# Kernel tuning notes

Hardware: AMD Instinct MI355X
Metric: run time of the kernel (lower is better)

The kernel has to match this reference:

```python
import jax, jax.numpy as jnp
import numpy as np

B, N, T = 2, 207, 864
L = 12           # patch_size
D = 96           # embed_dim
EPS = 1e-8
TAU = 1.0


def setup_inputs() -> dict:
    key = jax.random.key(0)
    k1, k2, k3, k4, k5 = jax.random.split(key, 5)
    return {
        "long_term_history": jax.random.normal(k1, (B, N, 1, T), dtype=jnp.float32),
        "adj_mx": jax.random.uniform(k2, (N, N), dtype=jnp.float32),
        "uniform_noise": jax.random.uniform(k3, (N, N), dtype=jnp.float32),
        "conv_weight": jax.random.normal(k4, (D, N, L), dtype=jnp.float32) * 0.02,
        "conv_bias": jax.random.normal(k5, (D,), dtype=jnp.float32) * 0.02,
        "k": 10,
    }


def _sample_k_neighbor_soft(adj_mx, uniform_noise, k):
    n = adj_mx.shape[0]
    logits = jnp.log(jax.nn.relu(adj_mx) + EPS)
    gumbel = -jnp.log(-jnp.log(uniform_noise + EPS))
    soft = jax.nn.softmax((logits + gumbel) / TAU, axis=1)          # [N, N]
    _, topk_idx = jax.lax.top_k(soft, k)                             # [N, k]
    hard = jnp.zeros_like(soft).at[jnp.arange(n)[:, None], topk_idx].set(1.0)
    return soft * hard                                               # [N, N]


def reference(long_term_history, adj_mx, uniform_noise, conv_weight, conv_bias, k):
    b, n, _, t = long_term_history.shape
    p = t // L
    mask = _sample_k_neighbor_soft(adj_mx, uniform_noise, k)         # [N, N]
    # expanded_history[b,i,j,t] = x[b,i,0,t]; neighbors = mask[i,j] * x[b,i,0,t]
    x = long_term_history[:, :, 0, :]                                # [B, N, T]
    neighbors = mask[None, :, :, None] * x[:, :, None, :]            # [B, N, N, T] (dense blow-up, as in source)
    xp = neighbors.reshape(b, n, n, p, L)                            # split T -> P patches of length L
    # Conv2d(N -> D, kernel (L,1), stride (L,1)) == contraction over (neighbor channel j, in-patch l)
    out = jnp.einsum('bijpl,djl->bidp', xp, conv_weight) + conv_bias[None, None, :, None]
    return out                                                       # [B, N, D, P]
```

## Files before the change

kernel.cpp:

```cpp
#include <hip/hip_runtime.h>
#include <math.h>

#define NN 207
#define BB 2
#define TT 864
#define LL 12
#define DD 96
#define PP 72
#define EPSF 1e-8f

__global__ __launch_bounds__(256) void stpe_fused_kernel(
    const float* __restrict__ x,
    const float* __restrict__ adj,
    const float* __restrict__ noise,
    const float* __restrict__ W,
    const float* __restrict__ bias,
    const int*   __restrict__ kptr,
    float*       __restrict__ out)
{
    __shared__ float s_score[NN];
    __shared__ float s_x[BB][TT];
    __shared__ float s_weff[DD * LL];
    __shared__ float s_bias[DD];
    __shared__ float s_topS[32];
    __shared__ int   s_topI[32];

    const int i   = blockIdx.x;
    const int tid = threadIdx.x;
    const int kk  = min(*kptr, 32);

    if (tid < NN) {
        float a = fmaxf(adj[i * NN + tid], 0.0f) + EPSF;
        float u = noise[i * NN + tid] + EPSF;
        s_score[tid] = logf(a) - logf(-logf(u));
    }
    if (tid < DD) s_bias[tid] = bias[tid];

    {
        const float4* x4  = (const float4*)x;
        float4*       sx4 = (float4*)&s_x[0][0];
        for (int q = tid; q < BB * (TT / 4); q += 256) {
            int b = q / (TT / 4), r = q - b * (TT / 4);
            sx4[q] = x4[(b * NN + i) * (TT / 4) + r];
        }
    }
    __syncthreads();

    if (tid < 64) {
        const int lane = tid;
        float v[4], orig[4];
        #pragma unroll
        for (int q = 0; q < 4; ++q) {
            int c = lane + 64 * q;
            v[q] = (c < NN) ? s_score[c] : -INFINITY;
            orig[q] = v[q];
        }
        float m = 0.0f, myv = 0.0f; int myi = 0;
        for (int it = 0; it < kk; ++it) {
            float bv = v[0]; int bi = lane;
            #pragma unroll
            for (int q = 1; q < 4; ++q)
                if (v[q] > bv) { bv = v[q]; bi = lane + 64 * q; }
            #pragma unroll
            for (int off = 32; off > 0; off >>= 1) {
                float ov = __shfl_xor(bv, off);
                int   oi = __shfl_xor(bi, off);
                if (ov > bv || (ov == bv && oi < bi)) { bv = ov; bi = oi; }
            }
            if (it == 0) m = bv;
            if (lane == it) { myv = bv; myi = bi; }
            if ((bi & 63) == lane) v[bi >> 6] = -INFINITY;
        }
        float se = 0.0f;
        #pragma unroll
        for (int q = 0; q < 4; ++q) {
            int c = lane + 64 * q;
            if (c < NN) se += expf(orig[q] - m);
        }
        #pragma unroll
        for (int off = 32; off > 0; off >>= 1) se += __shfl_xor(se, off);
        if (lane < kk) {
            s_topS[lane] = expf(myv - m) / se;
            s_topI[lane] = myi;
        }
    }
    __syncthreads();

    {
        const float4* W4 = (const float4*)W;
        float4* weff4 = (float4*)s_weff;
        for (int e = tid; e < DD * 3; e += 256) {
            int d = e / 3, c = e - d * 3;
            float4 acc = {0.f, 0.f, 0.f, 0.f};
            for (int t = 0; t < kk; ++t) {
                float s  = s_topS[t];
                float4 w = W4[(d * NN + s_topI[t]) * 3 + c];
                acc.x += s * w.x; acc.y += s * w.y;
                acc.z += s * w.z; acc.w += s * w.w;
            }
            weff4[e] = acc;
        }
    }
    __syncthreads();

    {
        float4* out4 = (float4*)out;
        for (int e = tid; e < BB * DD * (PP / 4); e += 256) {
            int b = e / (DD * (PP / 4));
            int r = e - b * (DD * (PP / 4));
            int d = r / (PP / 4);
            int c = r - d * (PP / 4);
            int p0 = c * 4;
            const float* wr = &s_weff[d * LL];
            float bd = s_bias[d];
            float o[4];
            #pragma unroll
            for (int q = 0; q < 4; ++q) {
                const float* xr = &s_x[b][(p0 + q) * LL];
                float a = bd;
                #pragma unroll
                for (int l = 0; l < LL; ++l) a += xr[l] * wr[l];
                o[q] = a;
            }
            float4 val = {o[0], o[1], o[2], o[3]};
            out4[((b * NN + i) * DD + d) * (PP / 4) + c] = val;
        }
    }
}

extern "C" void kernel_launch(void* const* d_in, const int* in_sizes, int n_in,
                              void* d_out, int out_size, void* d_ws, size_t ws_size,
                              hipStream_t stream) {
    const float* x     = (const float*)d_in[0];
    const float* adj   = (const float*)d_in[1];
    const float* noise = (const float*)d_in[2];
    const float* W     = (const float*)d_in[3];
    const float* bias  = (const float*)d_in[4];
    const int*   kptr  = (const int*)d_in[5];
    float* out = (float*)d_out;

    stpe_fused_kernel<<<NN, 256, 0, stream>>>(x, adj, noise, W, bias, kptr, out);
}
```

Before: 85.00 us.

## Split fused kernel into weff computation and fully parallel output kernel

Splits the single 207-block fused kernel into two launches. The first computes the top-k mixed effective weights per node and writes them to workspace. The second is an elementwise-parallel kernel, one thread per output float4, that reads x and weff directly from global memory. This spreads the 11 MB output write across many more blocks than the original 207, which underfilled the GPU's compute units. The cost is an extra launch, a global round trip for weff, and repeated x reads that now rely on the cache rather than LDS.

```diff
diff --git a/kernel.cpp b/kernel.cpp
--- a/kernel.cpp
+++ b/kernel.cpp
@@ -9,19 +9,14 @@
 #define PP 72
 #define EPSF 1e-8f
 
-__global__ __launch_bounds__(256) void stpe_fused_kernel(
-    const float* __restrict__ x,
+__global__ __launch_bounds__(256) void weff_kernel(
     const float* __restrict__ adj,
     const float* __restrict__ noise,
     const float* __restrict__ W,
-    const float* __restrict__ bias,
     const int*   __restrict__ kptr,
-    float*       __restrict__ out)
+    float*       __restrict__ weff)
 {
     __shared__ float s_score[NN];
-    __shared__ float s_x[BB][TT];
-    __shared__ float s_weff[DD * LL];
-    __shared__ float s_bias[DD];
     __shared__ float s_topS[32];
     __shared__ int   s_topI[32];
 
@@ -33,16 +28,6 @@
         float a = fmaxf(adj[i * NN + tid], 0.0f) + EPSF;
         float u = noise[i * NN + tid] + EPSF;
         s_score[tid] = logf(a) - logf(-logf(u));
-    }
-    if (tid < DD) s_bias[tid] = bias[tid];
-
-    {
-        const float4* x4  = (const float4*)x;
-        float4*       sx4 = (float4*)&s_x[0][0];
-        for (int q = tid; q < BB * (TT / 4); q += 256) {
-            int b = q / (TT / 4), r = q - b * (TT / 4);
-            sx4[q] = x4[(b * NN + i) * (TT / 4) + r];
-        }
     }
     __syncthreads();
 
@@ -87,8 +72,8 @@
     __syncthreads();
 
     {
-        const float4* W4 = (const float4*)W;
-        float4* weff4 = (float4*)s_weff;
+        const float4* W4  = (const float4*)W;
+        float4*       wf4 = (float4*)weff + i * (DD * 3);
         for (int e = tid; e < DD * 3; e += 256) {
             int d = e / 3, c = e - d * 3;
             float4 acc = {0.f, 0.f, 0.f, 0.f};
@@ -98,34 +83,47 @@
                 acc.x += s * w.x; acc.y += s * w.y;
                 acc.z += s * w.z; acc.w += s * w.w;
             }
-            weff4[e] = acc;
+            wf4[e] = acc;
         }
     }
-    __syncthreads();
+}
 
-    {
-        float4* out4 = (float4*)out;
-        for (int e = tid; e < BB * DD * (PP / 4); e += 256) {
-            int b = e / (DD * (PP / 4));
-            int r = e - b * (DD * (PP / 4));
-            int d = r / (PP / 4);
-            int c = r - d * (PP / 4);
-            int p0 = c * 4;
-            const float* wr = &s_weff[d * LL];
-            float bd = s_bias[d];
-            float o[4];
-            #pragma unroll
-            for (int q = 0; q < 4; ++q) {
-                const float* xr = &s_x[b][(p0 + q) * LL];
-                float a = bd;
-                #pragma unroll
-                for (int l = 0; l < LL; ++l) a += xr[l] * wr[l];
-                o[q] = a;
-            }
-            float4 val = {o[0], o[1], o[2], o[3]};
-            out4[((b * NN + i) * DD + d) * (PP / 4) + c] = val;
-        }
+__global__ __launch_bounds__(256) void out_kernel(
+    const float* __restrict__ x,
+    const float* __restrict__ weff,
+    const float* __restrict__ bias,
+    float*       __restrict__ out)
+{
+    const unsigned TOTAL = BB * NN * DD * (PP / 4);
+    unsigned e = blockIdx.x * 256u + threadIdx.x;
+    if (e >= TOTAL) return;
+
+    unsigned c  = e % 18u;
+    unsigned r  = e / 18u;
+    unsigned d  = r % (unsigned)DD;
+    unsigned bi = r / (unsigned)DD;
+    unsigned i  = bi % (unsigned)NN;
+
+    const float4* x4 = (const float4*)x + (size_t)bi * (TT / 4) + c * 12u;
+    const float4* w4 = (const float4*)weff + ((size_t)i * DD + d) * 3u;
+
+    float4 w0 = w4[0], w1 = w4[1], w2 = w4[2];
+    float  bd = bias[d];
+
+    float o[4];
+    #pragma unroll
+    for (int q = 0; q < 4; ++q) {
+        float4 a0 = x4[q * 3 + 0];
+        float4 a1 = x4[q * 3 + 1];
+        float4 a2 = x4[q * 3 + 2];
+        float s = bd;
+        s += a0.x * w0.x; s += a0.y * w0.y; s += a0.z * w0.z; s += a0.w * w0.w;
+        s += a1.x * w1.x; s += a1.y * w1.y; s += a1.z * w1.z; s += a1.w * w1.w;
+        s += a2.x * w2.x; s += a2.y * w2.y; s += a2.z * w2.z; s += a2.w * w2.w;
+        o[q] = s;
     }
+    float4 val = {o[0], o[1], o[2], o[3]};
+    ((float4*)out)[e] = val;
 }
 
 extern "C" void kernel_launch(void* const* d_in, const int* in_sizes, int n_in,
@@ -137,7 +135,11 @@
     const float* W     = (const float*)d_in[3];
     const float* bias  = (const float*)d_in[4];
     const int*   kptr  = (const int*)d_in[5];
-    float* out = (float*)d_out;
+    float* out  = (float*)d_out;
+    float* weff = (float*)d_ws;
 
-    stpe_fused_kernel<<<NN, 256, 0, stream>>>(x, adj, noise, W, bias, kptr, out);
+    weff_kernel<<<NN, 256, 0, stream>>>(adj, noise, W, kptr, weff);
+
+    const int total4 = BB * NN * DD * (PP / 4);
+    out_kernel<<<(total4 + 255) / 256, 256, 0, stream>>>(x, weff, bias, out);
 }
```

Measured after the change: 87.68 us. 3.2% more time.
